# Kernel optimization log

Measured on AMD Instinct MI355X. Metric: run time of the kernel, lower is better.

The kernel has to match this reference:

```python
import jax, jax.numpy as jnp
import numpy as np
import math

HEADS = 8
DIM_HEAD = 64
BATCH = 2
SEQ = 2048
KNN = 32
ATTN_SCALE_INIT = 20.0


def l2norm(t, eps=1e-12):
    n = jnp.sqrt(jnp.sum(t * t, axis=-1, keepdims=True))
    return t / jnp.maximum(n, eps)


def setup_inputs() -> dict:
    key = jax.random.key(0)
    ks = jax.random.split(key, 5)
    q = jax.random.normal(ks[0], (BATCH, HEADS, SEQ, DIM_HEAD), dtype=jnp.float32)
    k = jax.random.normal(ks[1], (BATCH, SEQ, DIM_HEAD), dtype=jnp.float32)
    v = jax.random.normal(ks[2], (BATCH, SEQ, DIM_HEAD), dtype=jnp.float32)
    scale_param = jnp.full((HEADS, 1, 1), math.log(ATTN_SCALE_INIT), dtype=jnp.float32)
    mem_kv = jax.random.normal(ks[3], (BATCH, HEADS, SEQ, KNN, 2, DIM_HEAD), dtype=jnp.float32)
    mask = jnp.ones((BATCH, SEQ), dtype=jnp.float32)
    mem_mask = jax.random.randint(ks[4], (BATCH, HEADS, SEQ, KNN), 0, 2).astype(jnp.bool_)
    return {"q": q, "k": k, "v": v, "scale_param": scale_param,
            "mem_kv": mem_kv, "mask": mask, "mem_mask": mem_mask}


def reference(q, k, v, scale_param, mem_kv, mask, mem_mask):
    neg = -jnp.finfo(q.dtype).max
    qn = l2norm(q)
    kn = l2norm(k)
    scale = jnp.exp(scale_param)  # [h,1,1]

    # local attention scores: [b,h,i,j]
    sim = jnp.einsum('bhid,bjd->bhij', qn, kn) * scale
    # key padding mask
    sim = sim + neg * (1.0 - mask[:, None, None, :])
    # causal mask (use_causal_mask=True), i == j here
    i, j = sim.shape[-2], sim.shape[-1]
    causal = jnp.triu(jnp.ones((i, j), dtype=jnp.bool_), j - i + 1)
    sim = jnp.where(causal, neg, sim)

    # memory branch: mem_kv [b,h,i,knn,2,d]
    mem_k = mem_kv[..., 0, :]
    mem_v = mem_kv[..., 1, :]
    sim_mem = jnp.einsum('bhid,bhijd->bhij', qn, mem_k) * scale
    sim_mem = jnp.where(mem_mask, sim_mem, neg)

    # joint softmax over [mem | local]
    full = jnp.concatenate((sim_mem, sim), axis=-1)
    attn = jax.nn.softmax(full, axis=-1)

    knn = mem_mask.shape[-1]
    mem_attn = attn[..., :knn]
    local_attn = attn[..., knn:]

    local_out = jnp.einsum('bhij,bjd->bhid', local_attn, v)
    mem_out = jnp.einsum('bhij,bhijd->bhid', mem_attn, mem_v)
    return local_out + mem_out
```

## Files before the change

### kernel.cpp

```cpp
#include <hip/hip_runtime.h>
#include <float.h>

#define HEADS 8
#define DIM 64
#define BATCH 2
#define SEQ 2048
#define KNN 32
#define QT 32
#define KT 64
#define NEGF (-3.402823466e38f)

typedef float f32x4 __attribute__((ext_vector_type(4)));
typedef __bf16 bf16x8 __attribute__((ext_vector_type(8)));

union F4 { float4 v; f32x4 e; float f[4]; };
union S8 { bf16x8 b; unsigned int u[4]; unsigned short us[8]; uint4 u4; uint2 u2[2]; };

__device__ __forceinline__ unsigned short f2bf(float x) {
    unsigned int u = __float_as_uint(x);
    u = (u + 0x7fffu + ((u >> 16) & 1u)) >> 16;
    return (unsigned short)u;
}


__global__ __launch_bounds__(256) void prep_kernel(const float* __restrict__ k,
                                                   const float* __restrict__ v,
                                                   const unsigned char* __restrict__ mmraw,
                                                   unsigned short* __restrict__ knBt,
                                                   unsigned short* __restrict__ vTt,
                                                   int* __restrict__ flag) {
    __shared__ float kn_s[64][65];
    __shared__ float vt_s[64][65];
    const int w = threadIdx.x >> 6, lane = threadIdx.x & 63;
    const int s0 = blockIdx.x * 64;
    const int b = s0 >> 11;
    const int s64 = (s0 & 2047) >> 6;
    for (int rr = 0; rr < 16; rr++) {
        const int sl = w * 16 + rr;
        const int row = s0 + sl;
        float kv = k[(size_t)row * DIM + lane];
        float ssq = kv * kv;
        #pragma unroll
        for (int m = 1; m < 64; m <<= 1) ssq += __shfl_xor(ssq, m);
        kn_s[sl][lane] = kv / fmaxf(sqrtf(ssq), 1e-12f);
        vt_s[sl][lane] = v[(size_t)row * DIM + lane];
    }
    __syncthreads();
    #pragma unroll
    for (int i = 0; i < 2; i++) {
        const int ch = threadIdx.x * 2 + i;
        const int s16g = ch >> 7;
        const int rem = ch & 127;
        const int rowc = rem >> 3;
        const int kc = (rem >> 2) & 1;
        const int oct = rem & 3;
        const float* src = &kn_s[s16g * 16 + rowc][kc * 32 + oct * 8];
        unsigned short tmp[8];
        #pragma unroll
        for (int e = 0; e < 8; e++) tmp[e] = f2bf(src[e]);
        const int s16 = s64 * 4 + s16g;
        unsigned short* dst = knBt + (((size_t)(b * 128 + s16) * 2 + kc) << 9)
                            + rowc * 32 + oct * 8;
        *(uint4*)dst = *(uint4*)&tmp[0];
    }
    #pragma unroll
    for (int i = 0; i < 2; i++) {
        const int ch = threadIdx.x * 2 + i;
        const int kk2 = ch >> 8;
        const int mtd = (ch >> 6) & 3;
        const int cc = (ch >> 2) & 15;
        const int q = ch & 3;
        unsigned short tmp[8];
        #pragma unroll
        for (int e = 0; e < 8; e++)
            tmp[e] = f2bf(vt_s[kk2 * 32 + q * 8 + e][mtd * 16 + cc]);
        unsigned short* dst = vTt + (((size_t)(b * 32 + s64) * 8 + kk2 * 4 + mtd) << 9)
                            + cc * 32 + q * 8;
        *(uint4*)dst = *(uint4*)&tmp[0];
    }
    if (blockIdx.x == 0 && w == 0) {
        int bad = 0;
        #pragma unroll
        for (int t = 0; t < 8; t++) {
            int idx = t * 64 + lane;
            if ((idx & 3) != 0 && mmraw[idx] != 0) bad = 1;
        }
        unsigned long long anybad = __ballot(bad);
        if (lane == 0) flag[0] = (anybad == 0ULL) ? 1 : 0;
    }
}

__global__ __launch_bounds__(256, 4) void mem_kernel(
    const float* __restrict__ q,
    const float* __restrict__ scale_param,
    const float* __restrict__ mem_kv,
    const void*  __restrict__ mem_mask,
    const int*   __restrict__ flagp,
    unsigned short* __restrict__ qnB,
    float* __restrict__ maccG,
    float* __restrict__ mG,
    float* __restrict__ lG)
{
    __shared__ float qn_s[4][64];
    __shared__ float p_s[4][32];
    const int w = threadIdx.x >> 6, lane = threadIdx.x & 63;
    const int mask_is_int = flagp[0];
    const int gid = blockIdx.x * 4 + w;
    const float scale = __expf(scale_param[(gid >> 11) & 7]);
    const float* rowp = mem_kv + (size_t)gid * (KNN * 2 * DIM);

    const int j1 = lane & 31, dh = lane >> 5;
    bool mybit;
    {
        size_t mmrow = (size_t)gid * KNN;
        mybit = mask_is_int ? (((const int*)mem_mask)[mmrow + j1] != 0)
                            : (((const unsigned char*)mem_mask)[mmrow + j1] != 0);
    }
    const unsigned int mb = (unsigned int)__ballot(mybit);

    float qv = q[(size_t)gid * DIM + lane];

    F4 dk[8];
    #pragma unroll
    for (int i = 0; i < 8; i++) dk[i].e = 0.f;
    {
        const float* kbase = rowp + j1 * (2 * DIM) + dh * 32;
        if (mybit) {
            #pragma unroll
            for (int i = 0; i < 8; i++) dk[i].e = *(const f32x4*)(kbase + 4 * i);
        }
    }
    const int g = lane >> 4, c16 = lane & 15;
    F4 dv[8];
    #pragma unroll
    for (int t = 0; t < 8; t++) {
        dv[t].e = 0.f;
        const int j2 = 4 * t + g;
        if ((mb >> j2) & 1u)
            dv[t].e = *(const f32x4*)(rowp + j2 * (2 * DIM) + DIM + c16 * 4);
    }

    float ssq = qv * qv;
    #pragma unroll
    for (int m2 = 1; m2 < 64; m2 <<= 1) ssq += __shfl_xor(ssq, m2);
    float qn = qv / fmaxf(sqrtf(ssq), 1e-12f);
    qnB[(size_t)gid * DIM + lane] = f2bf(qn);
    qn_s[w][lane] = qn;

    float s = 0.f;
    #pragma unroll
    for (int i = 0; i < 8; i++) {
        F4 qq; qq.v = *(const float4*)&qn_s[w][dh * 32 + 4 * i];
        s += dk[i].f[0] * qq.f[0] + dk[i].f[1] * qq.f[1]
           + dk[i].f[2] * qq.f[2] + dk[i].f[3] * qq.f[3];
    }
    s += __shfl_xor(s, 32);
    s = mybit ? s * scale : NEGF;

    float mx = s;
    #pragma unroll
    for (int m2 = 1; m2 < 32; m2 <<= 1) mx = fmaxf(mx, __shfl_xor(mx, m2));
    float p = __expf(s - mx);
    float ls = p;
    #pragma unroll
    for (int m2 = 1; m2 < 32; m2 <<= 1) ls += __shfl_xor(ls, m2);
    if (lane < 32) p_s[w][lane] = p;

    f32x4 acc = 0.f;
    #pragma unroll
    for (int t = 0; t < 8; t++) {
        float pv = p_s[w][4 * t + g];
        #pragma unroll
        for (int e = 0; e < 4; e++) acc[e] += pv * dv[t].f[e];
    }
    #pragma unroll
    for (int e = 0; e < 4; e++) {
        acc[e] += __shfl_xor(acc[e], 16);
        acc[e] += __shfl_xor(acc[e], 32);
    }
    if (g == 0) {
        F4 o; o.e = acc;
        *(float4*)(maccG + (size_t)gid * DIM + c16 * 4) = o.v;
    }
    if (lane == 0) { mG[gid] = mx; lG[gid] = ls; }
}

__global__ __launch_bounds__(256) void flash_kernel(
    const float* __restrict__ scale_param,
    const float* __restrict__ mask,
    const unsigned short* __restrict__ knBt,
    const unsigned short* __restrict__ vTt,
    const unsigned short* __restrict__ qnB,
    const float* __restrict__ maccG,
    const float* __restrict__ mG,
    const float* __restrict__ lG,
    float* __restrict__ out)
{
    __shared__ float maccs[QT][DIM + 4];
    __shared__ float mmem_s[QT], lmem_s[QT];
    __shared__ __attribute__((aligned(16))) unsigned short fragbuf[4][2][2][4][17][8];
    __shared__ float corr_s[4][QT];
    __shared__ float mlw[4][2][QT];
    __shared__ float linv_s[QT];

    const int tid = threadIdx.x;
    const int w = tid >> 6;
    const int lane = tid & 63;
    const int g = lane >> 4;
    const int c = lane & 15;
    const int bid = blockIdx.x;
    const int qt = 63 - (bid & 63);
    const int bh = bid >> 6;
    const int b = bh >> 3;
    const int h = bh & 7;
    const int i0 = qt * QT;
    const float scale = __expf(scale_param[h]);

    bf16x8 qa[2][2];
    #pragma unroll
    for (int mt = 0; mt < 2; mt++)
        #pragma unroll
        for (int kc = 0; kc < 2; kc++) {
            S8 t;
            t.u4 = *(const uint4*)(qnB + ((size_t)bh * SEQ + i0 + mt * 16 + c) * DIM + kc * 32 + g * 8);
            qa[mt][kc] = t.b;
        }

    f32x4 oacc[4][2];
    #pragma unroll
    for (int mtd = 0; mtd < 4; mtd++)
        #pragma unroll
        for (int ni = 0; ni < 2; ni++)
            #pragma unroll
            for (int r = 0; r < 4; r++) oacc[mtd][ni][r] = 0.f;
    float mrow[2] = {NEGF, NEGF}, lrow[2] = {0.f, 0.f};

    const int nkt = ((i0 + QT - 1) >> 6) + 1;
    const unsigned short* knTb = knBt + ((size_t)b * 128 * 2 << 9);
    const unsigned short* vTtb = vTt  + ((size_t)b * 32 * 8 << 9);
    const int lofs = c * 32;

    for (int jt = w; jt < nkt; jt += 4) {
        const int jb = jt * KT;

        bf16x8 va[4][2];
        #pragma unroll
        for (int mtd = 0; mtd < 4; mtd++)
            #pragma unroll
            for (int kk2 = 0; kk2 < 2; kk2++) {
                const unsigned short* vbase = vTtb + (((size_t)jt * 8 + kk2 * 4 + mtd) << 9) + lofs;
                S8 t;
                t.u2[0] = *(const uint2*)(vbase + 4 * g);
                t.u2[1] = *(const uint2*)(vbase + 16 + 4 * g);
                va[mtd][kk2] = t.b;
            }

        f32x4 sacc[2][4];
        #pragma unroll
        for (int mt = 0; mt < 2; mt++)
            #pragma unroll
            for (int nt = 0; nt < 4; nt++)
                #pragma unroll
                for (int r = 0; r < 4; r++) sacc[mt][nt][r] = 0.f;
        #pragma unroll
        for (int kc = 0; kc < 2; kc++) {
            #pragma unroll
            for (int nt = 0; nt < 4; nt++) {
                S8 kb;
                kb.u4 = *(const uint4*)(knTb + (((size_t)(jt * 4 + nt) * 2 + kc) << 9) + lofs + g * 8);
                #pragma unroll
                for (int mt = 0; mt < 2; mt++)
                    sacc[mt][nt] = __builtin_amdgcn_mfma_f32_16x16x32_bf16(kb.b, qa[mt][kc], sacc[mt][nt], 0, 0, 0);
            }
        }

        F4 mskv[4];
        #pragma unroll
        for (int nt = 0; nt < 4; nt++)
            mskv[nt].v = *(const float4*)(mask + b * SEQ + jb + nt * 16 + 4 * g);
        const bool docausal = (jb + 63 > i0);

        #pragma unroll
        for (int mt = 0; mt < 2; mt++) {
            const int iq = i0 + mt * 16 + c;
            float tm = NEGF;
            #pragma unroll
            for (int nt = 0; nt < 4; nt++)
                #pragma unroll
                for (int r = 0; r < 4; r++) {
                    float s = sacc[mt][nt][r] * scale + NEGF * (1.f - mskv[nt].f[r]);
                    if (docausal) {
                        int j = jb + nt * 16 + 4 * g + r;
                        if (j > iq) s = NEGF;
                    }
                    sacc[mt][nt][r] = s;
                    tm = fmaxf(tm, s);
                }
            tm = fmaxf(tm, __shfl_xor(tm, 16));
            tm = fmaxf(tm, __shfl_xor(tm, 32));
            float mnew = fmaxf(mrow[mt], tm);
            float corr = __expf(mrow[mt] - mnew);
            mrow[mt] = mnew;

            float ps = 0.f;
            #pragma unroll
            for (int nt = 0; nt < 4; nt++) {
                unsigned int lo, hi;
                float p0 = __expf(sacc[mt][nt][0] - mnew);
                float p1 = __expf(sacc[mt][nt][1] - mnew);
                float p2 = __expf(sacc[mt][nt][2] - mnew);
                float p3 = __expf(sacc[mt][nt][3] - mnew);
                ps += (p0 + p1) + (p2 + p3);
                lo = (unsigned int)f2bf(p0) | ((unsigned int)f2bf(p1) << 16);
                hi = (unsigned int)f2bf(p2) | ((unsigned int)f2bf(p3) << 16);
                *(uint2*)&fragbuf[w][mt][nt >> 1][g][c][4 * (nt & 1)] = make_uint2(lo, hi);
            }
            ps += __shfl_xor(ps, 16);
            ps += __shfl_xor(ps, 32);
            lrow[mt] = lrow[mt] * corr + ps;

            #pragma unroll
            for (int mtd = 0; mtd < 4; mtd++)
                #pragma unroll
                for (int r = 0; r < 4; r++) oacc[mtd][mt][r] *= corr;
        }

        #pragma unroll
        for (int kk2 = 0; kk2 < 2; kk2++)
            #pragma unroll
            for (int ni = 0; ni < 2; ni++) {
                S8 pb; pb.u4 = *(const uint4*)&fragbuf[w][ni][kk2][g][c][0];
                #pragma unroll
                for (int mtd = 0; mtd < 4; mtd++)
                    oacc[mtd][ni] = __builtin_amdgcn_mfma_f32_16x16x32_bf16(va[mtd][kk2], pb.b, oacc[mtd][ni], 0, 0, 0);
            }
    }

    {
        int i = tid >> 3, d0 = (tid & 7) * 8;
        const float* src = maccG + ((size_t)bh * SEQ + i0 + i) * DIM + d0;
        *(float4*)&maccs[i][d0]     = *(const float4*)src;
        *(float4*)&maccs[i][d0 + 4] = *(const float4*)(src + 4);
        if (tid < QT) {
            mmem_s[tid] = mG[(size_t)bh * SEQ + i0 + tid];
            lmem_s[tid] = lG[(size_t)bh * SEQ + i0 + tid];
        }
    }
    if (g == 0) {
        #pragma unroll
        for (int mt = 0; mt < 2; mt++) {
            mlw[w][0][mt * 16 + c] = mrow[mt];
            mlw[w][1][mt * 16 + c] = lrow[mt];
        }
    }
    __syncthreads();
    {
        int i = tid >> 3;
        int d0 = (tid & 7) * 8;
        float mM = mmem_s[i];
        #pragma unroll
        for (int w2 = 0; w2 < 4; w2++) mM = fmaxf(mM, mlw[w2][0][i]);
        float em = __expf(mmem_s[i] - mM);
        float L = lmem_s[i] * em;
        #pragma unroll
        for (int w2 = 0; w2 < 4; w2++) L += mlw[w2][1][i] * __expf(mlw[w2][0][i] - mM);
        #pragma unroll
        for (int e = 0; e < 8; e++) maccs[i][d0 + e] *= em;
        if ((tid & 7) == 0) linv_s[i] = 1.f / L;
        if ((tid & 7) == 1) corr_s[0][i] = mM;
    }
    __syncthreads();
    float ew0 = __expf(mlw[w][0][c]      - corr_s[0][c]);
    float ew1 = __expf(mlw[w][0][16 + c] - corr_s[0][16 + c]);
    for (int w2 = 0; w2 < 4; w2++) {
        if (w == w2) {
            #pragma unroll
            for (int mtd = 0; mtd < 4; mtd++)
                #pragma unroll
                for (int r = 0; r < 4; r++) {
                    maccs[c][mtd * 16 + 4 * g + r]      += oacc[mtd][0][r] * ew0;
                    maccs[16 + c][mtd * 16 + 4 * g + r] += oacc[mtd][1][r] * ew1;
                }
        }
        __syncthreads();
    }
    {
        int i = tid >> 3;
        int d0 = (tid & 7) * 8;
        float inv = linv_s[i];
        F4 o0, o1;
        o0.v = *(const float4*)&maccs[i][d0];
        o1.v = *(const float4*)&maccs[i][d0 + 4];
        #pragma unroll
        for (int e = 0; e < 4; e++) { o0.f[e] *= inv; o1.f[e] *= inv; }
        float* op = out + ((size_t)bh * SEQ + i0 + i) * DIM + d0;
        *(float4*)op = o0.v;
        *(float4*)(op + 4) = o1.v;
    }
}

extern "C" void kernel_launch(void* const* d_in, const int* in_sizes, int n_in,
                              void* d_out, int out_size, void* d_ws, size_t ws_size,
                              hipStream_t stream) {
    const float* q           = (const float*)d_in[0];
    const float* k           = (const float*)d_in[1];
    const float* v           = (const float*)d_in[2];
    const float* scale_param = (const float*)d_in[3];
    const float* mem_kv      = (const float*)d_in[4];
    const float* mask        = (const float*)d_in[5];
    const void*  mem_mask    = d_in[6];
    float* out = (float*)d_out;

    char* base = (char*)d_ws;
    int* flag            = (int*)base;
    unsigned short* knBt = (unsigned short*)(base + 1024);
    unsigned short* vTt  = (unsigned short*)(base + 1024 + (512ull << 10));
    unsigned short* qnB  = (unsigned short*)(base + 1024 + (1ull << 20));
    float* maccG         = (float*)(base + 1024 + (5ull << 20));
    float* mG            = (float*)(base + 1024 + (13ull << 20));
    float* lG            = (float*)(base + 1024 + (13ull << 20) + (256ull << 10));

    prep_kernel<<<dim3(BATCH * SEQ / 64), dim3(256), 0, stream>>>(
        k, v, (const unsigned char*)mem_mask, knBt, vTt, flag);
    mem_kernel<<<dim3(BATCH * HEADS * SEQ / 4), dim3(256), 0, stream>>>(
        q, scale_param, mem_kv, mem_mask, flag, qnB, maccG, mG, lG);
    flash_kernel<<<dim3(BATCH * HEADS * (SEQ / QT)), dim3(256), 0, stream>>>(
        scale_param, mask, knBt, vTt, qnB, maccG, mG, lG, out);
}
```

Baseline: 116.6 us.

## Restructure flash kernel: per-wave query rows, shared KV tiles with async double-buffering

Changes the flash kernel from splitting key tiles across waves (with a cross-wave softmax merge) to a 64-row query tile in which each wave owns 16 query rows and all waves sweep the same key/value tiles. Key and value fragments are staged into LDS through global_load_lds async copies and double-buffered, so the next tile loads while the current one is computed. The epilogue becomes a single per-row merge with the memory branch and no serialized per-wave accumulation. This removes redundant global loads and the multi-barrier merge, but halves the block count and adds a barrier on every key tile.

Measured after the change: 150.2 us. 1.29x slower.

```diff
diff --git a/kernel.cpp b/kernel.cpp
--- a/kernel.cpp
+++ b/kernel.cpp
@@ -6,7 +6,7 @@
 #define BATCH 2
 #define SEQ 2048
 #define KNN 32
-#define QT 32
+#define QT 64
 #define KT 64
 #define NEGF (-3.402823466e38f)
 
@@ -20,6 +20,12 @@
     unsigned int u = __float_as_uint(x);
     u = (u + 0x7fffu + ((u >> 16) & 1u)) >> 16;
     return (unsigned short)u;
+}
+
+__device__ __forceinline__ void async16u(const unsigned short* gsrc, unsigned short* ldst) {
+    __builtin_amdgcn_global_load_lds(
+        (const __attribute__((address_space(1))) unsigned int*)gsrc,
+        (__attribute__((address_space(3))) unsigned int*)ldst, 16, 0, 0);
 }
 
 
@@ -196,12 +202,11 @@
     const float* __restrict__ lG,
     float* __restrict__ out)
 {
-    __shared__ float maccs[QT][DIM + 4];
-    __shared__ float mmem_s[QT], lmem_s[QT];
-    __shared__ __attribute__((aligned(16))) unsigned short fragbuf[4][2][2][4][17][8];
-    __shared__ float corr_s[4][QT];
-    __shared__ float mlw[4][2][QT];
-    __shared__ float linv_s[QT];
+    __shared__ __attribute__((aligned(16))) unsigned short tiles[2][16][512];
+    __shared__ __attribute__((aligned(16))) unsigned short fragbuf[4][2][4][17][8];
+    __shared__ float bs_s[QT];
+
+    float* maccs = (float*)&tiles[0][0][0];
 
     const int tid = threadIdx.x;
     const int w = tid >> 6;
@@ -209,38 +214,52 @@
     const int g = lane >> 4;
     const int c = lane & 15;
     const int bid = blockIdx.x;
-    const int qt = 63 - (bid & 63);
-    const int bh = bid >> 6;
+    const int qt = 31 - (bid & 31);
+    const int bh = bid >> 5;
     const int b = bh >> 3;
     const int h = bh & 7;
     const int i0 = qt * QT;
     const float scale = __expf(scale_param[h]);
 
-    bf16x8 qa[2][2];
-    #pragma unroll
-    for (int mt = 0; mt < 2; mt++)
-        #pragma unroll
-        for (int kc = 0; kc < 2; kc++) {
-            S8 t;
-            t.u4 = *(const uint4*)(qnB + ((size_t)bh * SEQ + i0 + mt * 16 + c) * DIM + kc * 32 + g * 8);
-            qa[mt][kc] = t.b;
-        }
-
-    f32x4 oacc[4][2];
-    #pragma unroll
-    for (int mtd = 0; mtd < 4; mtd++)
-        #pragma unroll
-        for (int ni = 0; ni < 2; ni++)
-            #pragma unroll
-            for (int r = 0; r < 4; r++) oacc[mtd][ni][r] = 0.f;
-    float mrow[2] = {NEGF, NEGF}, lrow[2] = {0.f, 0.f};
-
-    const int nkt = ((i0 + QT - 1) >> 6) + 1;
     const unsigned short* knTb = knBt + ((size_t)b * 128 * 2 << 9);
     const unsigned short* vTtb = vTt  + ((size_t)b * 32 * 8 << 9);
-    const int lofs = c * 32;
-
-    for (int jt = w; jt < nkt; jt += 4) {
+
+    bf16x8 qa[2];
+    #pragma unroll
+    for (int kc = 0; kc < 2; kc++) {
+        S8 t;
+        t.u4 = *(const uint4*)(qnB + ((size_t)bh * SEQ + i0 + w * 16 + c) * DIM + kc * 32 + g * 8);
+        qa[kc] = t.b;
+    }
+
+    f32x4 oacc[4];
+    #pragma unroll
+    for (int mtd = 0; mtd < 4; mtd++)
+        #pragma unroll
+        for (int r = 0; r < 4; r++) oacc[mtd][r] = 0.f;
+    float mrow = NEGF, lrow = 0.f;
+
+    const int nkt = qt + 1;
+
+    #define STAGE(JT, BUF) {                                                         \
+        _Pragma("unroll")                                                            \
+        for (int fi = 0; fi < 4; fi++) {                                             \
+            const int fr = w * 4 + fi;                                               \
+            const unsigned short* src;                                               \
+            if (fr < 8)                                                              \
+                src = knTb + (((size_t)((JT) * 4 + (fr >> 1)) * 2 + (fr & 1)) << 9); \
+            else                                                                     \
+                src = vTtb + (((size_t)(JT) * 8 + (fr - 8)) << 9);                   \
+            async16u(src + (size_t)lane * 8, &tiles[BUF][fr][0]);                    \
+        }                                                                            \
+    }
+
+    STAGE(0, 0)
+    __syncthreads();
+
+    for (int jt = 0; jt < nkt; jt++) {
+        const int buf = jt & 1;
+        if (jt + 1 < nkt) STAGE(jt + 1, buf ^ 1)
         const int jb = jt * KT;
 
         bf16x8 va[4][2];
@@ -248,29 +267,25 @@
         for (int mtd = 0; mtd < 4; mtd++)
             #pragma unroll
             for (int kk2 = 0; kk2 < 2; kk2++) {
-                const unsigned short* vbase = vTtb + (((size_t)jt * 8 + kk2 * 4 + mtd) << 9) + lofs;
+                const unsigned short* vbase = &tiles[buf][8 + kk2 * 4 + mtd][0] + c * 32;
                 S8 t;
                 t.u2[0] = *(const uint2*)(vbase + 4 * g);
                 t.u2[1] = *(const uint2*)(vbase + 16 + 4 * g);
                 va[mtd][kk2] = t.b;
             }
 
-        f32x4 sacc[2][4];
-        #pragma unroll
-        for (int mt = 0; mt < 2; mt++)
-            #pragma unroll
-            for (int nt = 0; nt < 4; nt++)
-                #pragma unroll
-                for (int r = 0; r < 4; r++) sacc[mt][nt][r] = 0.f;
+        f32x4 sacc[4];
+        #pragma unroll
+        for (int nt = 0; nt < 4; nt++)
+            #pragma unroll
+            for (int r = 0; r < 4; r++) sacc[nt][r] = 0.f;
         #pragma unroll
         for (int kc = 0; kc < 2; kc++) {
             #pragma unroll
             for (int nt = 0; nt < 4; nt++) {
                 S8 kb;
-                kb.u4 = *(const uint4*)(knTb + (((size_t)(jt * 4 + nt) * 2 + kc) << 9) + lofs + g * 8);
-                #pragma unroll
-                for (int mt = 0; mt < 2; mt++)
-                    sacc[mt][nt] = __builtin_amdgcn_mfma_f32_16x16x32_bf16(kb.b, qa[mt][kc], sacc[mt][nt], 0, 0, 0);
+                kb.u4 = *(const uint4*)(&tiles[buf][nt * 2 + kc][0] + c * 32 + g * 8);
+                sacc[nt] = __builtin_amdgcn_mfma_f32_16x16x32_bf16(kb.b, qa[kc], sacc[nt], 0, 0, 0);
             }
         }
 
@@ -278,124 +293,99 @@
         #pragma unroll
         for (int nt = 0; nt < 4; nt++)
             mskv[nt].v = *(const float4*)(mask + b * SEQ + jb + nt * 16 + 4 * g);
-        const bool docausal = (jb + 63 > i0);
-
-        #pragma unroll
-        for (int mt = 0; mt < 2; mt++) {
-            const int iq = i0 + mt * 16 + c;
-            float tm = NEGF;
-            #pragma unroll
-            for (int nt = 0; nt < 4; nt++)
-                #pragma unroll
-                for (int r = 0; r < 4; r++) {
-                    float s = sacc[mt][nt][r] * scale + NEGF * (1.f - mskv[nt].f[r]);
-                    if (docausal) {
-                        int j = jb + nt * 16 + 4 * g + r;
-                        if (j > iq) s = NEGF;
-                    }
-                    sacc[mt][nt][r] = s;
-                    tm = fmaxf(tm, s);
+        const bool docausal = (jt == qt);
+
+        const int iq = i0 + w * 16 + c;
+        float tm = NEGF;
+        #pragma unroll
+        for (int nt = 0; nt < 4; nt++)
+            #pragma unroll
+            for (int r = 0; r < 4; r++) {
+                float s = sacc[nt][r] * scale + NEGF * (1.f - mskv[nt].f[r]);
+                if (docausal) {
+                    int j = jb + nt * 16 + 4 * g + r;
+                    if (j > iq) s = NEGF;
                 }
-            tm = fmaxf(tm, __shfl_xor(tm, 16));
-            tm = fmaxf(tm, __shfl_xor(tm, 32));
-            float mnew = fmaxf(mrow[mt], tm);
-            float corr = __expf(mrow[mt] - mnew);
-            mrow[mt] = mnew;
-
-            float ps = 0.f;
-            #pragma unroll
-            for (int nt = 0; nt < 4; nt++) {
-                unsigned int lo, hi;
-                float p0 = __expf(sacc[mt][nt][0] - mnew);
-                float p1 = __expf(sacc[mt][nt][1] - mnew);
-                float p2 = __expf(sacc[mt][nt][2] - mnew);
-                float p3 = __expf(sacc[mt][nt][3] - mnew);
-                ps += (p0 + p1) + (p2 + p3);
-                lo = (unsigned int)f2bf(p0) | ((unsigned int)f2bf(p1) << 16);
-                hi = (unsigned int)f2bf(p2) | ((unsigned int)f2bf(p3) << 16);
-                *(uint2*)&fragbuf[w][mt][nt >> 1][g][c][4 * (nt & 1)] = make_uint2(lo, hi);
+                sacc[nt][r] = s;
+                tm = fmaxf(tm, s);
             }
-            ps += __shfl_xor(ps, 16);
-            ps += __shfl_xor(ps, 32);
-            lrow[mt] = lrow[mt] * corr + ps;
-
+        tm = fmaxf(tm, __shfl_xor(tm, 16));
+        tm = fmaxf(tm, __shfl_xor(tm, 32));
+        float mnew = fmaxf(mrow, tm);
+        float corr = __expf(mrow - mnew);
+        mrow = mnew;
+
+        float ps = 0.f;
+        #pragma unroll
+        for (int nt = 0; nt < 4; nt++) {
+            float p0 = __expf(sacc[nt][0] - mnew);
+            float p1 = __expf(sacc[nt][1] - mnew);
+            float p2 = __expf(sacc[nt][2] - mnew);
+            float p3 = __expf(sacc[nt][3] - mnew);
+            ps += (p0 + p1) + (p2 + p3);
+            unsigned int lo = (unsigned int)f2bf(p0) | ((unsigned int)f2bf(p1) << 16);
+            unsigned int hi = (unsigned int)f2bf(p2) | ((unsigned int)f2bf(p3) << 16);
+            *(uint2*)&fragbuf[w][nt >> 1][g][c][4 * (nt & 1)] = make_uint2(lo, hi);
+        }
+        ps += __shfl_xor(ps, 16);
+        ps += __shfl_xor(ps, 32);
+        lrow = lrow * corr + ps;
+
+        #pragma unroll
+        for (int mtd = 0; mtd < 4; mtd++)
+            #pragma unroll
+            for (int r = 0; r < 4; r++) oacc[mtd][r] *= corr;
+
+        #pragma unroll
+        for (int kk2 = 0; kk2 < 2; kk2++) {
+            S8 pb; pb.u4 = *(const uint4*)&fragbuf[w][kk2][g][c][0];
             #pragma unroll
             for (int mtd = 0; mtd < 4; mtd++)
-                #pragma unroll
-                for (int r = 0; r < 4; r++) oacc[mtd][mt][r] *= corr;
-        }
-
-        #pragma unroll
-        for (int kk2 = 0; kk2 < 2; kk2++)
-            #pragma unroll
-            for (int ni = 0; ni < 2; ni++) {
-                S8 pb; pb.u4 = *(const uint4*)&fragbuf[w][ni][kk2][g][c][0];
-                #pragma unroll
-                for (int mtd = 0; mtd < 4; mtd++)
-                    oacc[mtd][ni] = __builtin_amdgcn_mfma_f32_16x16x32_bf16(va[mtd][kk2], pb.b, oacc[mtd][ni], 0, 0, 0);
-            }
-    }
+                oacc[mtd] = __builtin_amdgcn_mfma_f32_16x16x32_bf16(va[mtd][kk2], pb.b, oacc[mtd], 0, 0, 0);
+        }
+        __syncthreads();
+    }
+
+    const size_t rowg = (size_t)bh * SEQ + i0 + w * 16 + c;
+    float mmem = mG[rowg], lmem = lG[rowg];
+    float M = fmaxf(mrow, mmem);
+    float el = __expf(mrow - M);
+    float em = __expf(mmem - M);
+    float inv = 1.f / (lrow * el + lmem * em);
+    float acoef = el * inv;
+    if (g == 0) bs_s[w * 16 + c] = em * inv;
+    __syncthreads();
 
     {
-        int i = tid >> 3, d0 = (tid & 7) * 8;
-        const float* src = maccG + ((size_t)bh * SEQ + i0 + i) * DIM + d0;
-        *(float4*)&maccs[i][d0]     = *(const float4*)src;
-        *(float4*)&maccs[i][d0 + 4] = *(const float4*)(src + 4);
-        if (tid < QT) {
-            mmem_s[tid] = mG[(size_t)bh * SEQ + i0 + tid];
-            lmem_s[tid] = lG[(size_t)bh * SEQ + i0 + tid];
-        }
-    }
-    if (g == 0) {
-        #pragma unroll
-        for (int mt = 0; mt < 2; mt++) {
-            mlw[w][0][mt * 16 + c] = mrow[mt];
-            mlw[w][1][mt * 16 + c] = lrow[mt];
+        const int i = tid >> 2, d0c = (tid & 3) * 16;
+        const float bco = bs_s[i];
+        const float* src = maccG + ((size_t)bh * SEQ + i0 + i) * DIM + d0c;
+        #pragma unroll
+        for (int e = 0; e < 4; e++) {
+            F4 x; x.v = *(const float4*)(src + 4 * e);
+            #pragma unroll
+            for (int t2 = 0; t2 < 4; t2++) x.f[t2] *= bco;
+            *(float4*)&maccs[i * 68 + d0c + 4 * e] = x.v;
         }
     }
     __syncthreads();
     {
-        int i = tid >> 3;
-        int d0 = (tid & 7) * 8;
-        float mM = mmem_s[i];
-        #pragma unroll
-        for (int w2 = 0; w2 < 4; w2++) mM = fmaxf(mM, mlw[w2][0][i]);
-        float em = __expf(mmem_s[i] - mM);
-        float L = lmem_s[i] * em;
-        #pragma unroll
-        for (int w2 = 0; w2 < 4; w2++) L += mlw[w2][1][i] * __expf(mlw[w2][0][i] - mM);
-        #pragma unroll
-        for (int e = 0; e < 8; e++) maccs[i][d0 + e] *= em;
-        if ((tid & 7) == 0) linv_s[i] = 1.f / L;
-        if ((tid & 7) == 1) corr_s[0][i] = mM;
+        #pragma unroll
+        for (int mtd = 0; mtd < 4; mtd++) {
+            float* cell = &maccs[(w * 16 + c) * 68 + mtd * 16 + 4 * g];
+            F4 y; y.v = *(const float4*)cell;
+            #pragma unroll
+            for (int r = 0; r < 4; r++) y.f[r] += oacc[mtd][r] * acoef;
+            *(float4*)cell = y.v;
+        }
     }
     __syncthreads();
-    float ew0 = __expf(mlw[w][0][c]      - corr_s[0][c]);
-    float ew1 = __expf(mlw[w][0][16 + c] - corr_s[0][16 + c]);
-    for (int w2 = 0; w2 < 4; w2++) {
-        if (w == w2) {
-            #pragma unroll
-            for (int mtd = 0; mtd < 4; mtd++)
-                #pragma unroll
-                for (int r = 0; r < 4; r++) {
-                    maccs[c][mtd * 16 + 4 * g + r]      += oacc[mtd][0][r] * ew0;
-                    maccs[16 + c][mtd * 16 + 4 * g + r] += oacc[mtd][1][r] * ew1;
-                }
-        }
-        __syncthreads();
-    }
     {
-        int i = tid >> 3;
-        int d0 = (tid & 7) * 8;
-        float inv = linv_s[i];
-        F4 o0, o1;
-        o0.v = *(const float4*)&maccs[i][d0];
-        o1.v = *(const float4*)&maccs[i][d0 + 4];
-        #pragma unroll
-        for (int e = 0; e < 4; e++) { o0.f[e] *= inv; o1.f[e] *= inv; }
-        float* op = out + ((size_t)bh * SEQ + i0 + i) * DIM + d0;
-        *(float4*)op = o0.v;
-        *(float4*)(op + 4) = o1.v;
+        const int i = tid >> 2, d0c = (tid & 3) * 16;
+        float* op = out + ((size_t)bh * SEQ + i0 + i) * DIM + d0c;
+        #pragma unroll
+        for (int e = 0; e < 4; e++)
+            *(float4*)(op + 4 * e) = *(const float4*)&maccs[i * 68 + d0c + 4 * e];
     }
 }
 
```
